# Kernel tuning notes

Hardware: AMD Instinct MI355X
Metric: run time of the kernel (lower is better)

## Reference

```python
import jax, jax.numpy as jnp
import numpy as np
import math

B, NX, NY = 8, 1024, 1024
DIM_X = DIM_Y = DIM = 1024
H = 8


def layer_norm(x, g, b, eps=1e-5):
    mu = jnp.mean(x, axis=-1, keepdims=True)
    var = jnp.mean(jnp.square(x - mu), axis=-1, keepdims=True)
    return (x - mu) * jax.lax.rsqrt(var + eps) * g + b


def setup_inputs() -> dict:
    key = jax.random.key(0)
    ks = jax.random.split(key, 12)
    s = 1.0 / math.sqrt(DIM)
    return {
        "X": jax.random.normal(ks[0], (B, NX, DIM_X), jnp.float32),
        "Y": jax.random.normal(ks[1], (B, NY, DIM_Y), jnp.float32),
        "mask": jax.random.bernoulli(ks[2], 0.1, (B, NY)),  # True = masked out
        "Wq": jax.random.normal(ks[3], (DIM_X, DIM), jnp.float32) * s,
        "bq": jnp.zeros((DIM,), jnp.float32),
        "Wk": jax.random.normal(ks[4], (DIM_Y, DIM), jnp.float32) * s,
        "bk": jnp.zeros((DIM,), jnp.float32),
        "Wv": jax.random.normal(ks[5], (DIM_Y, DIM), jnp.float32) * s,
        "bv": jnp.zeros((DIM,), jnp.float32),
        "Wo": jax.random.normal(ks[6], (DIM, DIM), jnp.float32) * s,
        "bo": jnp.zeros((DIM,), jnp.float32),
        "g1": jnp.ones((DIM,), jnp.float32),
        "b1": jnp.zeros((DIM,), jnp.float32),
        "g2": jnp.ones((DIM,), jnp.float32),
        "b2": jnp.zeros((DIM,), jnp.float32),
    }


def reference(X, Y, mask, Wq, bq, Wk, bk, Wv, bv, Wo, bo, g1, b1, g2, b2):
    Q = X @ Wq + bq            # [B, NX, DIM]
    K = Y @ Wk + bk            # [B, NY, DIM]
    V = Y @ Wv + bv            # [B, NY, DIM]
    Dh = DIM // H
    Qh = Q.reshape(B, NX, H, Dh)
    Kh = K.reshape(B, NY, H, Dh)
    Vh = V.reshape(B, NY, H, Dh)
    # NOTE: original scales by sqrt(dim) (full model dim), not sqrt(head_dim)
    logits = jnp.einsum("bqhd,bkhd->bhqk", Qh, Kh) / math.sqrt(DIM)
    logits = jnp.where(mask[:, None, None, :], -jnp.inf, logits)
    A = jax.nn.softmax(logits, axis=-1)
    A = jnp.where(jnp.isnan(A), 0.0, A)  # fully-masked rows -> 0
    attn = jnp.einsum("bhqk,bkhd->bqhd", A, Vh).reshape(B, NX, DIM)
    O = layer_norm(Q + attn, g1, b1)
    O = layer_norm(O + jax.nn.relu(O @ Wo + bo), g2, b2)
    return O
```

## Files before the change

### kernel.cpp

```cpp
#include <hip/hip_runtime.h>
#include <stdint.h>


typedef unsigned short u16;
typedef unsigned int u32;
typedef __attribute__((ext_vector_type(8))) short s16x8;
typedef __attribute__((ext_vector_type(4))) float f32x4;
typedef __attribute__((ext_vector_type(16))) float f32x16;
typedef __attribute__((ext_vector_type(4))) u16 u16x4;

typedef __attribute__((address_space(1))) const void* as1cv;
typedef __attribute__((address_space(3))) void* as3v;

#define DEVINL __device__ __forceinline__

DEVINL u16 f2bf(float f) {
  union { float f; u32 u; } v; v.f = f;
  return (u16)((v.u + 0x7FFFu + ((v.u >> 16) & 1u)) >> 16);
}
DEVINL float bf2f(u16 x) {
  union { u32 u; float f; } v; v.u = ((u32)x) << 16;
  return v.f;
}
DEVINL u32 cvtpk_bf16(float lo, float hi) {
  u32 r;
  asm("v_cvt_pk_bf16_f32 %0, %1, %2" : "=v"(r) : "v"(lo), "v"(hi));
  return r;
}
DEVINL float fexp2(float x) {
  float r;
  asm("v_exp_f32 %0, %1" : "=v"(r) : "v"(x));
  return r;
}
DEVINL void gload_lds16(const void* g, void* l) {
  __builtin_amdgcn_global_load_lds((as1cv)g, (as3v)l, 16, 0, 0);
}
DEVINL f32x4 mfma16(s16x8 a, s16x8 b, f32x4 c) {
  return __builtin_amdgcn_mfma_f32_16x16x32_bf16(a, b, c, 0, 0, 0);
}
DEVINL f32x16 mfma32(s16x8 a, s16x8 b, f32x16 c) {
  return __builtin_amdgcn_mfma_f32_32x32x16_bf16(a, b, c, 0, 0, 0);
}

__global__ void prep_mask(const u32* __restrict__ mraw, float* __restrict__ maskb) {
  __shared__ int mode;
  int t = threadIdx.x;
  int fB = 0, fF = 0;
  for (int i = t; i < 2048; i += 256) {
    u32 v = mraw[i];
    if (v == 0x3F800000u) fF = 1;
    else if (v > 1u) fB = 1;
  }
  if (t == 0) mode = 0;
  __syncthreads();
  if (fB) atomicOr(&mode, 1);
  if (fF) atomicOr(&mode, 2);
  __syncthreads();
  int md = mode;
  int idx = blockIdx.x * 256 + t;
  int v;
  if (md & 1)       v = ((const unsigned char*)mraw)[idx] != 0;
  else if (md & 2)  v = ((const float*)mraw)[idx] != 0.0f;
  else              v = ((const int*)mraw)[idx] != 0;
  maskb[idx] = v ? -3e30f : -11.54156032f;
}

__global__ void cvt_f2bf2(const float* __restrict__ in0, u16* __restrict__ out0,
                          const float* __restrict__ in1, u16* __restrict__ out1,
                          int n4) {
  int i = blockIdx.x * blockDim.x + threadIdx.x;
  const float* in = in0;
  u16* out = out0;
  if (i >= n4) { i -= n4; in = in1; out = out1; }
  float4 v = *(const float4*)(in + (size_t)i * 4);
  u16x4 o; o[0] = f2bf(v.x); o[1] = f2bf(v.y); o[2] = f2bf(v.z); o[3] = f2bf(v.w);
  *(u16x4*)(out + (size_t)i * 4) = o;
}

__global__ void transpose_cvt(const float* __restrict__ W0, const float* __restrict__ W1,
                              const float* __restrict__ W2, const float* __restrict__ W3,
                              u16* __restrict__ T0, u16* __restrict__ T1,
                              u16* __restrict__ T2, u16* __restrict__ T3) {
  const float* W = (blockIdx.z == 0) ? W0 : (blockIdx.z == 1) ? W1 : (blockIdx.z == 2) ? W2 : W3;
  u16* T = (blockIdx.z == 0) ? T0 : (blockIdx.z == 1) ? T1 : (blockIdx.z == 2) ? T2 : T3;
  __shared__ float tile[32][33];
  int tx = threadIdx.x, ty = threadIdx.y;
  int N0 = blockIdx.x << 5, K0 = blockIdx.y << 5;
#pragma unroll
  for (int i = 0; i < 4; ++i)
    tile[ty + i * 8][tx] = W[(size_t)(K0 + ty + i * 8) * 1024 + N0 + tx];
  __syncthreads();
#pragma unroll
  for (int i = 0; i < 4; ++i)
    T[(size_t)(N0 + ty + i * 8) * 1024 + K0 + tx] = f2bf(tile[tx][ty + i * 8]);
}

template <int MODE>
__global__ __launch_bounds__(256, 2) void gemm_nt(
    const u16* __restrict__ A, const u16* __restrict__ Bt,
    const float* __restrict__ bias, float* __restrict__ outF,
    u16* __restrict__ outBF, const u16* __restrict__ residBF) {
  __shared__ u16 lA[128 * 64];
  __shared__ u16 lB[128 * 64];

  const int id = blockIdx.x;
  const int cpx = gridDim.x >> 3;
  const int swz = (id & 7) * cpx + (id >> 3);
  const int mb = swz >> 3;
  const int nb = swz & 7;

  const int tid = threadIdx.x;
  const int w = tid >> 6, l = tid & 63;
  const int wm = w >> 1, wn = w & 1;
  const int lrow = l & 15, lk = l >> 4;

  const int sr = l >> 3;
  const int scol = ((l & 7) << 4) ^ (sr << 4);
  const char* gA = (const char*)A + (size_t)(mb * 128) * 2048;
  const char* gB = (const char*)Bt + (size_t)(nb * 128) * 2048;

  f32x4 acc[4][4];
#pragma unroll
  for (int i = 0; i < 4; ++i)
#pragma unroll
    for (int j = 0; j < 4; ++j) acc[i][j] = f32x4{0.f, 0.f, 0.f, 0.f};

  for (int kt = 0; kt < 16; ++kt) {
    const int kb = kt * 128;
#pragma unroll
    for (int c = 0; c < 4; ++c) {
      int row = (w * 4 + c) * 8 + sr;
      gload_lds16(gA + (size_t)row * 2048 + kb + scol, (char*)lA + (w * 4 + c) * 1024);
      gload_lds16(gB + (size_t)row * 2048 + kb + scol, (char*)lB + (w * 4 + c) * 1024);
    }
    __syncthreads();
#pragma unroll
    for (int kc = 0; kc < 2; ++kc) {
      s16x8 af[4], bfr[4];
#pragma unroll
      for (int mi = 0; mi < 4; ++mi) {
        int row = wm * 64 + mi * 16 + lrow;
        int off = row * 128 + ((lk * 16 + kc * 64) ^ ((row & 7) << 4));
        af[mi] = *(const s16x8*)((const char*)lA + off);
      }
#pragma unroll
      for (int ni = 0; ni < 4; ++ni) {
        int row = wn * 64 + ni * 16 + lrow;
        int off = row * 128 + ((lk * 16 + kc * 64) ^ ((row & 7) << 4));
        bfr[ni] = *(const s16x8*)((const char*)lB + off);
      }
      __builtin_amdgcn_s_setprio(1);
#pragma unroll
      for (int mi = 0; mi < 4; ++mi)
#pragma unroll
        for (int ni = 0; ni < 4; ++ni)
          acc[mi][ni] = mfma16(af[mi], bfr[ni], acc[mi][ni]);
      __builtin_amdgcn_s_setprio(0);
    }
    __syncthreads();
  }

  const int growb = mb * 128 + wm * 64;
  const int gcolb = nb * 128 + wn * 64;
  float bs[4];
#pragma unroll
  for (int ni = 0; ni < 4; ++ni) bs[ni] = bias[gcolb + ni * 16 + lrow];

#pragma unroll
  for (int mi = 0; mi < 4; ++mi) {
    const int grow0 = growb + mi * 16 + lk * 4;
#pragma unroll
    for (int ni = 0; ni < 4; ++ni) {
      const int gcol = gcolb + ni * 16 + lrow;
      if (MODE == 2) {
        u16x4 pk;
#pragma unroll
        for (int r = 0; r < 4; ++r) pk[r] = f2bf(acc[mi][ni][r] + bs[ni]);
        size_t flat = ((size_t)((grow0 >> 10) << 10) + gcol) * 1024 + (grow0 & 1023);
        *(u16x4*)(outBF + flat) = pk;
      } else {
#pragma unroll
        for (int r = 0; r < 4; ++r) {
          float v = acc[mi][ni][r] + bs[ni];
          size_t idx = (size_t)(grow0 + r) * 1024 + gcol;
          if (MODE == 1) { outBF[idx] = f2bf(v); }
          if (MODE == 3) { outF[idx] = bf2f(residBF[idx]) + fmaxf(v, 0.f); }
        }
      }
    }
  }
}

__global__ __launch_bounds__(256, 2) void attn_fwd(
    const u16* __restrict__ Qbf, const u16* __restrict__ Kbf,
    const u16* __restrict__ Vt, const float* __restrict__ maskb,
    u16* __restrict__ attnO) {
  __shared__ u16 lK[128 * 128];
  __shared__ u16 lV[128 * 128];
  __shared__ float lM[1024];

  const int id = blockIdx.x;
  const int xcd = id & 7, seq = id >> 3;
  const int bh = xcd * 8 + (seq >> 3);
  const int qb = seq & 7;
  const int b = bh >> 3, h = bh & 7;
  const int tid = threadIdx.x;
  const int w = tid >> 6, l = tid & 63;
  const int q32 = l & 31, hi = l >> 5;

  const u16* Qrow = Qbf + ((size_t)(b * 1024 + qb * 128 + w * 32 + q32)) * 1024 + h * 128;
  s16x8 qf[8];
#pragma unroll
  for (int dc = 0; dc < 8; ++dc) qf[dc] = *(const s16x8*)(Qrow + dc * 16 + hi * 8);

  const char* gK = (const char*)(Kbf + ((size_t)(b * 1024)) * 1024 + h * 128);
  const char* gV = (const char*)(Vt + ((size_t)(b * 1024 + h * 128)) * 1024);
  const float* mrow = maskb + b * 1024;

  if (w == 0) {
#pragma unroll
    for (int c = 0; c < 4; ++c)
      gload_lds16(mrow + c * 256 + l * 4, (char*)lM + c * 1024);
  }

  float l_ = 0.f;
  f32x16 oacc[4];
#pragma unroll
  for (int i = 0; i < 4; ++i)
#pragma unroll
    for (int r = 0; r < 16; ++r) oacc[i][r] = 0.f;

  const int sr = l >> 4, slot = l & 15;
  const float SCL = 0.04508422f;

  for (int t = 0; t < 8; ++t) {
    const int kbase = t * 128;
#pragma unroll
    for (int c = 0; c < 8; ++c) {
      int row = (w * 8 + c) * 4 + sr;
      int scol = (slot << 4) ^ ((row & 15) << 4);
      gload_lds16(gK + (size_t)(kbase + row) * 2048 + scol, (char*)lK + (w * 8 + c) * 1024);
      gload_lds16(gV + (size_t)row * 2048 + kbase * 2 + scol, (char*)lV + (w * 8 + c) * 1024);
    }
    __syncthreads();

    f32x16 sc[4];
#pragma unroll
    for (int kb = 0; kb < 4; ++kb)
#pragma unroll
      for (int r = 0; r < 16; ++r) sc[kb][r] = 0.f;
    __builtin_amdgcn_s_setprio(1);
#pragma unroll
    for (int dc = 0; dc < 8; ++dc) {
#pragma unroll
      for (int kb = 0; kb < 4; ++kb) {
        int row = kb * 32 + q32;
        int off = row * 256 + ((dc * 32 + hi * 16) ^ ((row & 15) << 4));
        s16x8 kf = *(const s16x8*)((const char*)lK + off);
        sc[kb] = mfma32(kf, qf[dc], sc[kb]);
      }
    }
    __builtin_amdgcn_s_setprio(0);

    float rs = 0.f;
#pragma unroll
    for (int kb = 0; kb < 4; ++kb) {
      const char* lMb = (const char*)lM + (size_t)(kbase + kb * 32 + hi * 4) * 4;
      f32x4 mv0 = *(const f32x4*)(lMb + 0);
      f32x4 mv1 = *(const f32x4*)(lMb + 32);
      f32x4 mv2 = *(const f32x4*)(lMb + 64);
      f32x4 mv3 = *(const f32x4*)(lMb + 96);
#pragma unroll
      for (int r = 0; r < 16; ++r) {
        float mb_ = (r < 4) ? mv0[r & 3] : (r < 8) ? mv1[r & 3] : (r < 12) ? mv2[r & 3] : mv3[r & 3];
        float pe = fexp2(fmaf(sc[kb][r], SCL, mb_));
        sc[kb][r] = pe;
        rs += pe;
      }
    }
    rs += __shfl_xor(rs, 32);
    l_ += rs;

    u32 pk[4][8];
#pragma unroll
    for (int kb = 0; kb < 4; ++kb)
#pragma unroll
      for (int r2 = 0; r2 < 8; ++r2)
        pk[kb][r2] = cvtpk_bf16(sc[kb][2 * r2], sc[kb][2 * r2 + 1]);

#pragma unroll
    for (int kc = 0; kc < 8; ++kc) {
      const int kb = kc >> 1;
      const int ra = (kc & 1) * 4, rb = ra + 2;
      u32 E0 = hi ? pk[kb][ra + 0] : pk[kb][rb + 0];
      u32 E1 = hi ? pk[kb][ra + 1] : pk[kb][rb + 1];
      u32 G0 = __shfl_xor(E0, 32), G1 = __shfl_xor(E1, 32);
      u32 S0 = hi ? pk[kb][rb + 0] : pk[kb][ra + 0];
      u32 S1 = hi ? pk[kb][rb + 1] : pk[kb][ra + 1];
      union { u32 u[4]; s16x8 v; } pa;
      pa.u[0] = hi ? G0 : S0;
      pa.u[1] = hi ? G1 : S1;
      pa.u[2] = hi ? S0 : G0;
      pa.u[3] = hi ? S1 : G1;
      __builtin_amdgcn_s_setprio(1);
#pragma unroll
      for (int nb = 0; nb < 4; ++nb) {
        int row = nb * 32 + q32;
        int off = row * 256 + ((kc * 32 + hi * 16) ^ ((row & 15) << 4));
        s16x8 vb = *(const s16x8*)((const char*)lV + off);
        oacc[nb] = mfma32(pa.v, vb, oacc[nb]);
      }
      __builtin_amdgcn_s_setprio(0);
    }
    __syncthreads();
  }

  rs_done:;
  float inv = (l_ > 1e-20f) ? (1.0f / l_) : 0.f;
  u16* obase = attnO + ((size_t)(b * 1024 + qb * 128 + w * 32)) * 1024 + h * 128;
#pragma unroll
  for (int r = 0; r < 16; ++r) {
    int qr = (r & 3) + 8 * (r >> 2) + 4 * hi;
    float iv = __shfl(inv, qr);
#pragma unroll
    for (int nb = 0; nb < 4; ++nb)
      obase[(size_t)qr * 1024 + nb * 32 + q32] = f2bf(oacc[nb][r] * iv);
  }
}

__global__ __launch_bounds__(256) void ln_fused(
    const float* __restrict__ aF, const u16* __restrict__ aBF,
    const u16* __restrict__ baddBF, const float* __restrict__ g,
    const float* __restrict__ bt, float* __restrict__ outF,
    u16* __restrict__ outBF) {
  const int row = blockIdx.x;
  const int c = threadIdx.x << 2;
  const size_t base = (size_t)row * 1024 + c;
  float4 h;
  if (aF) {
    h = *(const float4*)(aF + base);
  } else {
    u16x4 u = *(const u16x4*)(aBF + base);
    h.x = bf2f(u[0]); h.y = bf2f(u[1]); h.z = bf2f(u[2]); h.w = bf2f(u[3]);
  }
  if (baddBF) {
    u16x4 u = *(const u16x4*)(baddBF + base);
    h.x += bf2f(u[0]); h.y += bf2f(u[1]); h.z += bf2f(u[2]); h.w += bf2f(u[3]);
  }
  float s = (h.x + h.y) + (h.z + h.w);
  float q = (h.x * h.x + h.y * h.y) + (h.z * h.z + h.w * h.w);
#pragma unroll
  for (int msk = 1; msk < 64; msk <<= 1) {
    s += __shfl_xor(s, msk);
    q += __shfl_xor(q, msk);
  }
  __shared__ float sh[8];
  const int w = threadIdx.x >> 6;
  if ((threadIdx.x & 63) == 0) { sh[w] = s; sh[4 + w] = q; }
  __syncthreads();
  s = (sh[0] + sh[1]) + (sh[2] + sh[3]);
  q = (sh[4] + sh[5]) + (sh[6] + sh[7]);
  const float mu = s * (1.f / 1024.f);
  const float var = q * (1.f / 1024.f) - mu * mu;
  const float rstd = rsqrtf(var + 1e-5f);
  const float4 gv = *(const float4*)(g + c);
  const float4 bv = *(const float4*)(bt + c);
  float4 o;
  o.x = (h.x - mu) * rstd * gv.x + bv.x;
  o.y = (h.y - mu) * rstd * gv.y + bv.y;
  o.z = (h.z - mu) * rstd * gv.z + bv.z;
  o.w = (h.w - mu) * rstd * gv.w + bv.w;
  if (outF) *(float4*)(outF + base) = o;
  if (outBF) {
    u16x4 ub; ub[0] = f2bf(o.x); ub[1] = f2bf(o.y); ub[2] = f2bf(o.z); ub[3] = f2bf(o.w);
    *(u16x4*)(outBF + base) = ub;
  }
}

extern "C" void kernel_launch(void* const* d_in, const int* in_sizes, int n_in,
                              void* d_out, int out_size, void* d_ws, size_t ws_size,
                              hipStream_t stream) {
  const float* X  = (const float*)d_in[0];
  const float* Y  = (const float*)d_in[1];
  const void*  mask = d_in[2];
  const float* Wq = (const float*)d_in[3];
  const float* bq = (const float*)d_in[4];
  const float* Wk = (const float*)d_in[5];
  const float* bk = (const float*)d_in[6];
  const float* Wv = (const float*)d_in[7];
  const float* bv = (const float*)d_in[8];
  const float* Wo = (const float*)d_in[9];
  const float* bo = (const float*)d_in[10];
  const float* g1 = (const float*)d_in[11];
  const float* b1 = (const float*)d_in[12];
  const float* g2 = (const float*)d_in[13];
  const float* b2 = (const float*)d_in[14];
  float* out = (float*)d_out;

  char* ws = (char*)d_ws;
  const size_t MB = 1024ull * 1024ull;
  u16* Xbf    = (u16*)(ws + 0);
  u16* Ybf    = (u16*)(ws + 16 * MB);
  u16* Qbf    = (u16*)(ws + 32 * MB);
  u16* Kbf    = (u16*)(ws + 48 * MB);
  u16* Vt     = (u16*)(ws + 64 * MB);
  u16* attnbf = (u16*)(ws + 80 * MB);
  u16* Wqt = (u16*)(ws + 112 * MB);
  u16* Wkt = (u16*)(ws + 114 * MB);
  u16* Wvt = (u16*)(ws + 116 * MB);
  u16* Wot = (u16*)(ws + 118 * MB);
  float* maskb = (float*)(ws + 120 * MB);
  float* R = (float*)(ws + 48 * MB);
  u16* O1bf = Xbf;

  prep_mask<<<dim3(32), dim3(256), 0, stream>>>((const u32*)mask, maskb);
  cvt_f2bf2<<<dim3(16384), dim3(256), 0, stream>>>(X, Xbf, Y, Ybf, 2097152);
  transpose_cvt<<<dim3(32, 32, 4), dim3(32, 8), 0, stream>>>(Wq, Wk, Wv, Wo, Wqt, Wkt, Wvt, Wot);

  gemm_nt<1><<<dim3(512), dim3(256), 0, stream>>>(Xbf, Wqt, bq, nullptr, Qbf, nullptr);
  gemm_nt<1><<<dim3(512), dim3(256), 0, stream>>>(Ybf, Wkt, bk, nullptr, Kbf, nullptr);
  gemm_nt<2><<<dim3(512), dim3(256), 0, stream>>>(Ybf, Wvt, bv, nullptr, Vt, nullptr);

  attn_fwd<<<dim3(512), dim3(256), 0, stream>>>(Qbf, Kbf, Vt, maskb, attnbf);

  ln_fused<<<dim3(8192), dim3(256), 0, stream>>>(nullptr, Qbf, attnbf, g1, b1, nullptr, O1bf);
  gemm_nt<3><<<dim3(512), dim3(256), 0, stream>>>(O1bf, Wot, bo, R, nullptr, O1bf);
  ln_fused<<<dim3(8192), dim3(256), 0, stream>>>(R, nullptr, nullptr, g2, b2, out, nullptr);
}
```

Before: 186.1 us.

## Double-buffer attention K/V tiles, use permlane32 swap, store residual in bf16

The attention kernel now splits each 128-key tile into two 64-key halves held in double-buffered LDS, so the load of the next half is issued before computing on the current one. Global and LDS offsets are precomputed once per thread. The shuffle-based P fragment exchange is replaced with v_permlane32_swap. Separately, the output-projection GEMM writes its residual+ReLU result as bf16 instead of fp32, which halves that intermediate's traffic at some cost in precision before the final layernorm.

New measurement: 182.9 us. No clear change (-1.7%).

```diff
diff --git a/kernel.cpp b/kernel.cpp
--- a/kernel.cpp
+++ b/kernel.cpp
@@ -184,7 +184,7 @@
           float v = acc[mi][ni][r] + bs[ni];
           size_t idx = (size_t)(grow0 + r) * 1024 + gcol;
           if (MODE == 1) { outBF[idx] = f2bf(v); }
-          if (MODE == 3) { outF[idx] = bf2f(residBF[idx]) + fmaxf(v, 0.f); }
+          if (MODE == 3) { outBF[idx] = f2bf(bf2f(residBF[idx]) + fmaxf(v, 0.f)); }
         }
       }
     }
@@ -195,8 +195,8 @@
     const u16* __restrict__ Qbf, const u16* __restrict__ Kbf,
     const u16* __restrict__ Vt, const float* __restrict__ maskb,
     u16* __restrict__ attnO) {
-  __shared__ u16 lK[128 * 128];
-  __shared__ u16 lV[128 * 128];
+  __shared__ u16 lK[2][64 * 128];
+  __shared__ u16 lV[2][128 * 64];
   __shared__ float lM[1024];
 
   const int id = blockIdx.x;
@@ -213,14 +213,31 @@
 #pragma unroll
   for (int dc = 0; dc < 8; ++dc) qf[dc] = *(const s16x8*)(Qrow + dc * 16 + hi * 8);
 
-  const char* gK = (const char*)(Kbf + ((size_t)(b * 1024)) * 1024 + h * 128);
-  const char* gV = (const char*)(Vt + ((size_t)(b * 1024 + h * 128)) * 1024);
-  const float* mrow = maskb + b * 1024;
+  const int srK = l >> 4, slK = l & 15;
+  const int srV = l >> 3, slV = l & 7;
+  int soK[4], soV[4];
+#pragma unroll
+  for (int c = 0; c < 4; ++c) {
+    int rowK = (w * 4 + c) * 4 + srK;
+    soK[c] = rowK * 2048 + ((slK << 4) ^ ((rowK & 15) << 4));
+    int dV = (w * 4 + c) * 8 + srV;
+    soV[c] = dV * 2048 + ((slV << 4) ^ ((dV & 7) << 4));
+  }
+  const char* pgK = (const char*)(Kbf + ((size_t)(b * 1024)) * 1024 + h * 128);
+  const char* pgV = (const char*)(Vt + ((size_t)(b * 1024 + h * 128)) * 1024);
+
+  int loK[8], loV[4];
+#pragma unroll
+  for (int c = 0; c < 8; ++c)
+    loK[c] = q32 * 256 + ((c * 32 + hi * 16) ^ ((q32 & 15) << 4));
+#pragma unroll
+  for (int c = 0; c < 4; ++c)
+    loV[c] = q32 * 128 + ((c * 32 + hi * 16) ^ ((q32 & 7) << 4));
 
   if (w == 0) {
 #pragma unroll
     for (int c = 0; c < 4; ++c)
-      gload_lds16(mrow + c * 256 + l * 4, (char*)lM + c * 1024);
+      gload_lds16(maskb + b * 1024 + c * 256 + l * 4, (char*)lM + c * 1024);
   }
 
   float l_ = 0.f;
@@ -230,92 +247,101 @@
 #pragma unroll
     for (int r = 0; r < 16; ++r) oacc[i][r] = 0.f;
 
-  const int sr = l >> 4, slot = l & 15;
   const float SCL = 0.04508422f;
 
-  for (int t = 0; t < 8; ++t) {
-    const int kbase = t * 128;
-#pragma unroll
-    for (int c = 0; c < 8; ++c) {
-      int row = (w * 8 + c) * 4 + sr;
-      int scol = (slot << 4) ^ ((row & 15) << 4);
-      gload_lds16(gK + (size_t)(kbase + row) * 2048 + scol, (char*)lK + (w * 8 + c) * 1024);
-      gload_lds16(gV + (size_t)row * 2048 + kbase * 2 + scol, (char*)lV + (w * 8 + c) * 1024);
-    }
+#define ATT_STAGE(NXT, TN)                                                    \
+  {                                                                           \
+    const char* pk_ = pgK + (size_t)(TN)*131072;                              \
+    const char* pv_ = pgV + (size_t)(TN)*128;                                 \
+    _Pragma("unroll")                                                         \
+    for (int c = 0; c < 4; ++c) {                                             \
+      gload_lds16(pk_ + soK[c], (char*)lK[NXT] + w * 4096 + c * 1024);        \
+      gload_lds16(pv_ + soV[c], (char*)lV[NXT] + w * 4096 + c * 1024);        \
+    }                                                                         \
+  }
+
+#define ATT_COMPUTE(CUR, PMT)                                                 \
+  {                                                                           \
+    f32x16 sc[2];                                                             \
+    _Pragma("unroll")                                                         \
+    for (int kb = 0; kb < 2; ++kb)                                            \
+      _Pragma("unroll")                                                       \
+      for (int r = 0; r < 16; ++r) sc[kb][r] = 0.f;                           \
+    __builtin_amdgcn_s_setprio(1);                                            \
+    _Pragma("unroll")                                                         \
+    for (int dc = 0; dc < 8; ++dc) {                                          \
+      _Pragma("unroll")                                                       \
+      for (int kb = 0; kb < 2; ++kb) {                                        \
+        s16x8 kf = *(const s16x8*)((const char*)lK[CUR] + loK[dc] + kb * 8192); \
+        sc[kb] = mfma32(kf, qf[dc], sc[kb]);                                  \
+      }                                                                       \
+    }                                                                         \
+    __builtin_amdgcn_s_setprio(0);                                            \
+    float rs = 0.f;                                                           \
+    _Pragma("unroll")                                                         \
+    for (int kb = 0; kb < 2; ++kb) {                                          \
+      f32x4 mv[4];                                                            \
+      _Pragma("unroll")                                                       \
+      for (int g = 0; g < 4; ++g)                                             \
+        mv[g] = *(const f32x4*)((PMT) + kb * 128 + g * 32);                   \
+      _Pragma("unroll")                                                       \
+      for (int r = 0; r < 16; ++r) {                                          \
+        float pe = fexp2(fmaf(sc[kb][r], SCL, mv[r >> 2][r & 3]));            \
+        sc[kb][r] = pe;                                                       \
+        rs += pe;                                                             \
+      }                                                                       \
+    }                                                                         \
+    rs += __shfl_xor(rs, 32);                                                 \
+    l_ += rs;                                                                 \
+    u32 pk[2][8];                                                             \
+    _Pragma("unroll")                                                         \
+    for (int kb = 0; kb < 2; ++kb)                                            \
+      _Pragma("unroll")                                                       \
+      for (int r2 = 0; r2 < 8; ++r2)                                          \
+        pk[kb][r2] = cvtpk_bf16(sc[kb][2 * r2], sc[kb][2 * r2 + 1]);          \
+    _Pragma("unroll")                                                         \
+    for (int kc = 0; kc < 4; ++kc) {                                          \
+      const int kb = kc >> 1;                                                 \
+      const int ra = (kc & 1) * 4;                                            \
+      u32 x0 = pk[kb][ra + 0], y0 = pk[kb][ra + 2];                           \
+      u32 x1 = pk[kb][ra + 1], y1 = pk[kb][ra + 3];                           \
+      asm("v_permlane32_swap_b32 %0, %1" : "+v"(x0), "+v"(y0));               \
+      asm("v_permlane32_swap_b32 %0, %1" : "+v"(x1), "+v"(y1));               \
+      union { u32 u[4]; s16x8 v; } pa;                                        \
+      pa.u[0] = x0; pa.u[1] = x1; pa.u[2] = y0; pa.u[3] = y1;                 \
+      __builtin_amdgcn_s_setprio(1);                                          \
+      _Pragma("unroll")                                                       \
+      for (int nb = 0; nb < 4; ++nb) {                                        \
+        s16x8 vb = *(const s16x8*)((const char*)lV[CUR] + loV[kc] + nb * 4096); \
+        oacc[nb] = mfma32(pa.v, vb, oacc[nb]);                                \
+      }                                                                       \
+      __builtin_amdgcn_s_setprio(0);                                          \
+    }                                                                         \
+  }
+
+  const char* pM0 = (const char*)lM + hi * 16;
+
+  ATT_STAGE(0, 0);
+  __syncthreads();
+  for (int it = 0; it < 7; ++it) {
+    const char* pMa = pM0 + it * 512;
+    ATT_STAGE(1, 2 * it + 1);
+    ATT_COMPUTE(0, pMa);
     __syncthreads();
-
-    f32x16 sc[4];
-#pragma unroll
-    for (int kb = 0; kb < 4; ++kb)
-#pragma unroll
-      for (int r = 0; r < 16; ++r) sc[kb][r] = 0.f;
-    __builtin_amdgcn_s_setprio(1);
-#pragma unroll
-    for (int dc = 0; dc < 8; ++dc) {
-#pragma unroll
-      for (int kb = 0; kb < 4; ++kb) {
-        int row = kb * 32 + q32;
-        int off = row * 256 + ((dc * 32 + hi * 16) ^ ((row & 15) << 4));
-        s16x8 kf = *(const s16x8*)((const char*)lK + off);
-        sc[kb] = mfma32(kf, qf[dc], sc[kb]);
-      }
-    }
-    __builtin_amdgcn_s_setprio(0);
-
-    float rs = 0.f;
-#pragma unroll
-    for (int kb = 0; kb < 4; ++kb) {
-      const char* lMb = (const char*)lM + (size_t)(kbase + kb * 32 + hi * 4) * 4;
-      f32x4 mv0 = *(const f32x4*)(lMb + 0);
-      f32x4 mv1 = *(const f32x4*)(lMb + 32);
-      f32x4 mv2 = *(const f32x4*)(lMb + 64);
-      f32x4 mv3 = *(const f32x4*)(lMb + 96);
-#pragma unroll
-      for (int r = 0; r < 16; ++r) {
-        float mb_ = (r < 4) ? mv0[r & 3] : (r < 8) ? mv1[r & 3] : (r < 12) ? mv2[r & 3] : mv3[r & 3];
-        float pe = fexp2(fmaf(sc[kb][r], SCL, mb_));
-        sc[kb][r] = pe;
-        rs += pe;
-      }
-    }
-    rs += __shfl_xor(rs, 32);
-    l_ += rs;
-
-    u32 pk[4][8];
-#pragma unroll
-    for (int kb = 0; kb < 4; ++kb)
-#pragma unroll
-      for (int r2 = 0; r2 < 8; ++r2)
-        pk[kb][r2] = cvtpk_bf16(sc[kb][2 * r2], sc[kb][2 * r2 + 1]);
-
-#pragma unroll
-    for (int kc = 0; kc < 8; ++kc) {
-      const int kb = kc >> 1;
-      const int ra = (kc & 1) * 4, rb = ra + 2;
-      u32 E0 = hi ? pk[kb][ra + 0] : pk[kb][rb + 0];
-      u32 E1 = hi ? pk[kb][ra + 1] : pk[kb][rb + 1];
-      u32 G0 = __shfl_xor(E0, 32), G1 = __shfl_xor(E1, 32);
-      u32 S0 = hi ? pk[kb][rb + 0] : pk[kb][ra + 0];
-      u32 S1 = hi ? pk[kb][rb + 1] : pk[kb][ra + 1];
-      union { u32 u[4]; s16x8 v; } pa;
-      pa.u[0] = hi ? G0 : S0;
-      pa.u[1] = hi ? G1 : S1;
-      pa.u[2] = hi ? S0 : G0;
-      pa.u[3] = hi ? S1 : G1;
-      __builtin_amdgcn_s_setprio(1);
-#pragma unroll
-      for (int nb = 0; nb < 4; ++nb) {
-        int row = nb * 32 + q32;
-        int off = row * 256 + ((kc * 32 + hi * 16) ^ ((row & 15) << 4));
-        s16x8 vb = *(const s16x8*)((const char*)lV + off);
-        oacc[nb] = mfma32(pa.v, vb, oacc[nb]);
-      }
-      __builtin_amdgcn_s_setprio(0);
-    }
+    ATT_STAGE(0, 2 * it + 2);
+    ATT_COMPUTE(1, pMa + 256);
     __syncthreads();
   }
-
-  rs_done:;
+  {
+    const char* pMa = pM0 + 7 * 512;
+    ATT_STAGE(1, 15);
+    ATT_COMPUTE(0, pMa);
+    __syncthreads();
+    ATT_COMPUTE(1, pMa + 256);
+  }
+#undef ATT_STAGE
+#undef ATT_COMPUTE
+
   float inv = (l_ > 1e-20f) ? (1.0f / l_) : 0.f;
   u16* obase = attnO + ((size_t)(b * 1024 + qb * 128 + w * 32)) * 1024 + h * 128;
 #pragma unroll
@@ -410,7 +436,7 @@
   u16* Wvt = (u16*)(ws + 116 * MB);
   u16* Wot = (u16*)(ws + 118 * MB);
   float* maskb = (float*)(ws + 120 * MB);
-  float* R = (float*)(ws + 48 * MB);
+  u16* Rbf = Kbf;
   u16* O1bf = Xbf;
 
   prep_mask<<<dim3(32), dim3(256), 0, stream>>>((const u32*)mask, maskb);
@@ -424,6 +450,6 @@
   attn_fwd<<<dim3(512), dim3(256), 0, stream>>>(Qbf, Kbf, Vt, maskb, attnbf);
 
   ln_fused<<<dim3(8192), dim3(256), 0, stream>>>(nullptr, Qbf, attnbf, g1, b1, nullptr, O1bf);
-  gemm_nt<3><<<dim3(512), dim3(256), 0, stream>>>(O1bf, Wot, bo, R, nullptr, O1bf);
-  ln_fused<<<dim3(8192), dim3(256), 0, stream>>>(R, nullptr, nullptr, g2, b2, out, nullptr);
-}
+  gemm_nt<3><<<dim3(512), dim3(256), 0, stream>>>(O1bf, Wot, bo, nullptr, Rbf, O1bf);
+  ln_fused<<<dim3(8192), dim3(256), 0, stream>>>(nullptr, Rbf, nullptr, g2, b2, out, nullptr);
+}
```

## Split attention over key halves with smaller tiles and combine in LN1

Applied to the files above, without the earlier changes.

The attention kernel now splits each query block's key range into two halves, one per workgroup. That doubles the grid to 1024 blocks, halves the LDS tiles, and raises the occupancy hint to 4 waves per SIMD. Each half writes its unnormalized output and row sums, and a new ln1_combine kernel merges them, normalizes, adds Q and applies the first layer norm. It also swaps the cross-half shuffle for v_permlane32_swap, precomputes LDS offsets, and stores the Wo-GEMM residual output in bf16 instead of fp32. The cost is extra global traffic for the two partial outputs, plus lower precision in the second layer norm input.

Result: slower. 242.0 us (+30.0%).

```diff
diff --git a/kernel.cpp b/kernel.cpp
--- a/kernel.cpp
+++ b/kernel.cpp
@@ -184,25 +184,26 @@
           float v = acc[mi][ni][r] + bs[ni];
           size_t idx = (size_t)(grow0 + r) * 1024 + gcol;
           if (MODE == 1) { outBF[idx] = f2bf(v); }
-          if (MODE == 3) { outF[idx] = bf2f(residBF[idx]) + fmaxf(v, 0.f); }
+          if (MODE == 3) { outBF[idx] = f2bf(bf2f(residBF[idx]) + fmaxf(v, 0.f)); }
         }
       }
     }
   }
 }
 
-__global__ __launch_bounds__(256, 2) void attn_fwd(
+__global__ __launch_bounds__(256, 4) void attn_fwd(
     const u16* __restrict__ Qbf, const u16* __restrict__ Kbf,
     const u16* __restrict__ Vt, const float* __restrict__ maskb,
-    u16* __restrict__ attnO) {
-  __shared__ u16 lK[128 * 128];
-  __shared__ u16 lV[128 * 128];
-  __shared__ float lM[1024];
+    u16* __restrict__ U, float* __restrict__ lsum) {
+  __shared__ u16 lK[64 * 128];
+  __shared__ u16 lV[128 * 64];
+  __shared__ float lM[512];
 
   const int id = blockIdx.x;
   const int xcd = id & 7, seq = id >> 3;
-  const int bh = xcd * 8 + (seq >> 3);
-  const int qb = seq & 7;
+  const int bh = xcd * 8 + (seq >> 4);
+  const int sub = seq & 15;
+  const int qb = sub >> 1, half = sub & 1;
   const int b = bh >> 3, h = bh & 7;
   const int tid = threadIdx.x;
   const int w = tid >> 6, l = tid & 63;
@@ -213,14 +214,31 @@
 #pragma unroll
   for (int dc = 0; dc < 8; ++dc) qf[dc] = *(const s16x8*)(Qrow + dc * 16 + hi * 8);
 
-  const char* gK = (const char*)(Kbf + ((size_t)(b * 1024)) * 1024 + h * 128);
-  const char* gV = (const char*)(Vt + ((size_t)(b * 1024 + h * 128)) * 1024);
-  const float* mrow = maskb + b * 1024;
+  const int srK = l >> 4, slK = l & 15;
+  const int srV = l >> 3, slV = l & 7;
+  int soK[4], soV[4];
+#pragma unroll
+  for (int c = 0; c < 4; ++c) {
+    int rowK = (w * 4 + c) * 4 + srK;
+    soK[c] = rowK * 2048 + ((slK << 4) ^ ((rowK & 15) << 4));
+    int dV = (w * 4 + c) * 8 + srV;
+    soV[c] = dV * 2048 + ((slV << 4) ^ ((dV & 7) << 4));
+  }
+  const char* pgK = (const char*)(Kbf + ((size_t)(b * 1024)) * 1024 + h * 128);
+  const char* pgV = (const char*)(Vt + ((size_t)(b * 1024 + h * 128)) * 1024);
+
+  int loK[8], loV[4];
+#pragma unroll
+  for (int c = 0; c < 8; ++c)
+    loK[c] = q32 * 256 + ((c * 32 + hi * 16) ^ ((q32 & 15) << 4));
+#pragma unroll
+  for (int c = 0; c < 4; ++c)
+    loV[c] = q32 * 128 + ((c * 32 + hi * 16) ^ ((q32 & 7) << 4));
 
   if (w == 0) {
 #pragma unroll
-    for (int c = 0; c < 4; ++c)
-      gload_lds16(mrow + c * 256 + l * 4, (char*)lM + c * 1024);
+    for (int c = 0; c < 2; ++c)
+      gload_lds16(maskb + b * 1024 + half * 512 + c * 256 + l * 4, (char*)lM + c * 1024);
   }
 
   float l_ = 0.f;
@@ -230,50 +248,50 @@
 #pragma unroll
     for (int r = 0; r < 16; ++r) oacc[i][r] = 0.f;
 
-  const int sr = l >> 4, slot = l & 15;
   const float SCL = 0.04508422f;
-
-  for (int t = 0; t < 8; ++t) {
-    const int kbase = t * 128;
-#pragma unroll
-    for (int c = 0; c < 8; ++c) {
-      int row = (w * 8 + c) * 4 + sr;
-      int scol = (slot << 4) ^ ((row & 15) << 4);
-      gload_lds16(gK + (size_t)(kbase + row) * 2048 + scol, (char*)lK + (w * 8 + c) * 1024);
-      gload_lds16(gV + (size_t)row * 2048 + kbase * 2 + scol, (char*)lV + (w * 8 + c) * 1024);
+  const char* pM0 = (const char*)lM + hi * 16;
+  const int tbase = half * 8;
+
+  for (int t8 = 0; t8 < 8; ++t8) {
+    const int t = tbase + t8;
+    {
+      const char* pk_ = pgK + (size_t)t * 131072;
+      const char* pv_ = pgV + (size_t)t * 128;
+#pragma unroll
+      for (int c = 0; c < 4; ++c) {
+        gload_lds16(pk_ + soK[c], (char*)lK + w * 4096 + c * 1024);
+        gload_lds16(pv_ + soV[c], (char*)lV + w * 4096 + c * 1024);
+      }
     }
     __syncthreads();
 
-    f32x16 sc[4];
-#pragma unroll
-    for (int kb = 0; kb < 4; ++kb)
+    f32x16 sc[2];
+#pragma unroll
+    for (int kb = 0; kb < 2; ++kb)
 #pragma unroll
       for (int r = 0; r < 16; ++r) sc[kb][r] = 0.f;
     __builtin_amdgcn_s_setprio(1);
 #pragma unroll
     for (int dc = 0; dc < 8; ++dc) {
 #pragma unroll
-      for (int kb = 0; kb < 4; ++kb) {
-        int row = kb * 32 + q32;
-        int off = row * 256 + ((dc * 32 + hi * 16) ^ ((row & 15) << 4));
-        s16x8 kf = *(const s16x8*)((const char*)lK + off);
+      for (int kb = 0; kb < 2; ++kb) {
+        s16x8 kf = *(const s16x8*)((const char*)lK + loK[dc] + kb * 8192);
         sc[kb] = mfma32(kf, qf[dc], sc[kb]);
       }
     }
     __builtin_amdgcn_s_setprio(0);
 
+    const char* pMa = pM0 + t8 * 256;
     float rs = 0.f;
 #pragma unroll
-    for (int kb = 0; kb < 4; ++kb) {
-      const char* lMb = (const char*)lM + (size_t)(kbase + kb * 32 + hi * 4) * 4;
-      f32x4 mv0 = *(const f32x4*)(lMb + 0);
-      f32x4 mv1 = *(const f32x4*)(lMb + 32);
-      f32x4 mv2 = *(const f32x4*)(lMb + 64);
-      f32x4 mv3 = *(const f32x4*)(lMb + 96);
+    for (int kb = 0; kb < 2; ++kb) {
+      f32x4 mv[4];
+#pragma unroll
+      for (int g = 0; g < 4; ++g)
+        mv[g] = *(const f32x4*)(pMa + kb * 128 + g * 32);
 #pragma unroll
       for (int r = 0; r < 16; ++r) {
-        float mb_ = (r < 4) ? mv0[r & 3] : (r < 8) ? mv1[r & 3] : (r < 12) ? mv2[r & 3] : mv3[r & 3];
-        float pe = fexp2(fmaf(sc[kb][r], SCL, mb_));
+        float pe = fexp2(fmaf(sc[kb][r], SCL, mv[r >> 2][r & 3]));
         sc[kb][r] = pe;
         rs += pe;
       }
@@ -281,33 +299,27 @@
     rs += __shfl_xor(rs, 32);
     l_ += rs;
 
-    u32 pk[4][8];
-#pragma unroll
-    for (int kb = 0; kb < 4; ++kb)
+    u32 pk[2][8];
+#pragma unroll
+    for (int kb = 0; kb < 2; ++kb)
 #pragma unroll
       for (int r2 = 0; r2 < 8; ++r2)
         pk[kb][r2] = cvtpk_bf16(sc[kb][2 * r2], sc[kb][2 * r2 + 1]);
 
 #pragma unroll
-    for (int kc = 0; kc < 8; ++kc) {
+    for (int kc = 0; kc < 4; ++kc) {
       const int kb = kc >> 1;
-      const int ra = (kc & 1) * 4, rb = ra + 2;
-      u32 E0 = hi ? pk[kb][ra + 0] : pk[kb][rb + 0];
-      u32 E1 = hi ? pk[kb][ra + 1] : pk[kb][rb + 1];
-      u32 G0 = __shfl_xor(E0, 32), G1 = __shfl_xor(E1, 32);
-      u32 S0 = hi ? pk[kb][rb + 0] : pk[kb][ra + 0];
-      u32 S1 = hi ? pk[kb][rb + 1] : pk[kb][ra + 1];
+      const int ra = (kc & 1) * 4;
+      u32 x0 = pk[kb][ra + 0], y0 = pk[kb][ra + 2];
+      u32 x1 = pk[kb][ra + 1], y1 = pk[kb][ra + 3];
+      asm("v_permlane32_swap_b32 %0, %1" : "+v"(x0), "+v"(y0));
+      asm("v_permlane32_swap_b32 %0, %1" : "+v"(x1), "+v"(y1));
       union { u32 u[4]; s16x8 v; } pa;
-      pa.u[0] = hi ? G0 : S0;
-      pa.u[1] = hi ? G1 : S1;
-      pa.u[2] = hi ? S0 : G0;
-      pa.u[3] = hi ? S1 : G1;
+      pa.u[0] = x0; pa.u[1] = x1; pa.u[2] = y0; pa.u[3] = y1;
       __builtin_amdgcn_s_setprio(1);
 #pragma unroll
       for (int nb = 0; nb < 4; ++nb) {
-        int row = nb * 32 + q32;
-        int off = row * 256 + ((kc * 32 + hi * 16) ^ ((row & 15) << 4));
-        s16x8 vb = *(const s16x8*)((const char*)lV + off);
+        s16x8 vb = *(const s16x8*)((const char*)lV + loV[kc] + nb * 4096);
         oacc[nb] = mfma32(pa.v, vb, oacc[nb]);
       }
       __builtin_amdgcn_s_setprio(0);
@@ -315,17 +327,63 @@
     __syncthreads();
   }
 
-  rs_done:;
-  float inv = (l_ > 1e-20f) ? (1.0f / l_) : 0.f;
-  u16* obase = attnO + ((size_t)(b * 1024 + qb * 128 + w * 32)) * 1024 + h * 128;
+  if (hi == 0)
+    lsum[half * 65536 + bh * 1024 + qb * 128 + w * 32 + q32] = l_;
+  u16* ubase = U + (size_t)half * 8388608 +
+               ((size_t)(b * 1024 + qb * 128 + w * 32)) * 1024 + h * 128;
 #pragma unroll
   for (int r = 0; r < 16; ++r) {
     int qr = (r & 3) + 8 * (r >> 2) + 4 * hi;
-    float iv = __shfl(inv, qr);
 #pragma unroll
     for (int nb = 0; nb < 4; ++nb)
-      obase[(size_t)qr * 1024 + nb * 32 + q32] = f2bf(oacc[nb][r] * iv);
-  }
+      ubase[(size_t)qr * 1024 + nb * 32 + q32] = f2bf(oacc[nb][r]);
+  }
+}
+
+__global__ __launch_bounds__(256) void ln1_combine(
+    const u16* __restrict__ Qbf, const u16* __restrict__ U,
+    const float* __restrict__ lsum, const float* __restrict__ g,
+    const float* __restrict__ bt, u16* __restrict__ outBF) {
+  const int row = blockIdx.x;
+  const int c = threadIdx.x << 2;
+  const size_t base = (size_t)row * 1024 + c;
+  const int b = row >> 10, qx = row & 1023;
+  const int hh = c >> 7;
+  const int li = (b * 8 + hh) * 1024 + qx;
+  const float lt = lsum[li] + lsum[65536 + li];
+  const float inv = (lt > 1e-20f) ? (1.0f / lt) : 0.f;
+  u16x4 uq = *(const u16x4*)(Qbf + base);
+  u16x4 u0 = *(const u16x4*)(U + base);
+  u16x4 u1 = *(const u16x4*)(U + 8388608 + base);
+  float4 h;
+  h.x = bf2f(uq[0]) + (bf2f(u0[0]) + bf2f(u1[0])) * inv;
+  h.y = bf2f(uq[1]) + (bf2f(u0[1]) + bf2f(u1[1])) * inv;
+  h.z = bf2f(uq[2]) + (bf2f(u0[2]) + bf2f(u1[2])) * inv;
+  h.w = bf2f(uq[3]) + (bf2f(u0[3]) + bf2f(u1[3])) * inv;
+  float s = (h.x + h.y) + (h.z + h.w);
+  float q = (h.x * h.x + h.y * h.y) + (h.z * h.z + h.w * h.w);
+#pragma unroll
+  for (int msk = 1; msk < 64; msk <<= 1) {
+    s += __shfl_xor(s, msk);
+    q += __shfl_xor(q, msk);
+  }
+  __shared__ float sh[8];
+  const int w = threadIdx.x >> 6;
+  if ((threadIdx.x & 63) == 0) { sh[w] = s; sh[4 + w] = q; }
+  __syncthreads();
+  s = (sh[0] + sh[1]) + (sh[2] + sh[3]);
+  q = (sh[4] + sh[5]) + (sh[6] + sh[7]);
+  const float mu = s * (1.f / 1024.f);
+  const float var = q * (1.f / 1024.f) - mu * mu;
+  const float rstd = rsqrtf(var + 1e-5f);
+  const float4 gv = *(const float4*)(g + c);
+  const float4 bv = *(const float4*)(bt + c);
+  u16x4 ub;
+  ub[0] = f2bf((h.x - mu) * rstd * gv.x + bv.x);
+  ub[1] = f2bf((h.y - mu) * rstd * gv.y + bv.y);
+  ub[2] = f2bf((h.z - mu) * rstd * gv.z + bv.z);
+  ub[3] = f2bf((h.w - mu) * rstd * gv.w + bv.w);
+  *(u16x4*)(outBF + base) = ub;
 }
 
 __global__ __launch_bounds__(256) void ln_fused(
@@ -404,13 +462,14 @@
   u16* Qbf    = (u16*)(ws + 32 * MB);
   u16* Kbf    = (u16*)(ws + 48 * MB);
   u16* Vt     = (u16*)(ws + 64 * MB);
-  u16* attnbf = (u16*)(ws + 80 * MB);
+  u16* Ubf    = (u16*)(ws + 80 * MB);
   u16* Wqt = (u16*)(ws + 112 * MB);
   u16* Wkt = (u16*)(ws + 114 * MB);
   u16* Wvt = (u16*)(ws + 116 * MB);
   u16* Wot = (u16*)(ws + 118 * MB);
   float* maskb = (float*)(ws + 120 * MB);
-  float* R = (float*)(ws + 48 * MB);
+  float* lsum  = (float*)(ws + 16 * MB);
+  u16* Rbf = Kbf;
   u16* O1bf = Xbf;
 
   prep_mask<<<dim3(32), dim3(256), 0, stream>>>((const u32*)mask, maskb);
@@ -421,9 +480,9 @@
   gemm_nt<1><<<dim3(512), dim3(256), 0, stream>>>(Ybf, Wkt, bk, nullptr, Kbf, nullptr);
   gemm_nt<2><<<dim3(512), dim3(256), 0, stream>>>(Ybf, Wvt, bv, nullptr, Vt, nullptr);
 
-  attn_fwd<<<dim3(512), dim3(256), 0, stream>>>(Qbf, Kbf, Vt, maskb, attnbf);
-
-  ln_fused<<<dim3(8192), dim3(256), 0, stream>>>(nullptr, Qbf, attnbf, g1, b1, nullptr, O1bf);
-  gemm_nt<3><<<dim3(512), dim3(256), 0, stream>>>(O1bf, Wot, bo, R, nullptr, O1bf);
-  ln_fused<<<dim3(8192), dim3(256), 0, stream>>>(R, nullptr, nullptr, g2, b2, out, nullptr);
-}
+  attn_fwd<<<dim3(1024), dim3(256), 0, stream>>>(Qbf, Kbf, Vt, maskb, Ubf, lsum);
+
+  ln1_combine<<<dim3(8192), dim3(256), 0, stream>>>(Qbf, Ubf, lsum, g1, b1, O1bf);
+  gemm_nt<3><<<dim3(512), dim3(256), 0, stream>>>(O1bf, Wot, bo, nullptr, Rbf, O1bf);
+  ln_fused<<<dim3(8192), dim3(256), 0, stream>>>(nullptr, Rbf, nullptr, g2, b2, out, nullptr);
+}
```
